# Optimization experiments

Measured on AMD Instinct MI355X. Metric: run time of the kernel, lower is better.

## Reference

```python
import jax, jax.numpy as jnp
import numpy as np

SOBEL_X = jnp.array([[-1., 0., 1.], [-2., 0., 2.], [-1., 0., 1.]], dtype=jnp.float32)
LAP = jnp.array([[1., 2., 1.], [2., -12., 2.], [1., 2., 1.]], dtype=jnp.float32)
UPDATE_RATE = 0.5


def _perchannel_conv(x, filters):
    # x: [B,C,H,W]; filters: [F,3,3]; circular pad, depthwise conv with F outputs per channel
    B, C, H, W = x.shape
    Fk = filters.shape[0]
    xp = jnp.pad(x, ((0, 0), (0, 0), (1, 1), (1, 1)), mode='wrap')
    # kernel[c*Fk + f] = filters[f] -> output channel order [c0f0,c0f1,c0f2,c1f0,...] matching torch reshape
    k = jnp.broadcast_to(filters[None], (C, Fk, 3, 3)).reshape(C * Fk, 1, 3, 3)
    return jax.lax.conv_general_dilated(xp, k, (1, 1), 'VALID',
                                        feature_group_count=C,
                                        dimension_numbers=('NCHW', 'OIHW', 'NCHW'))


def _unfold27(x):
    # circular pad over (C,H,W) then gather the 27-neighborhood: [B,C,H,W] -> [B,C,27,H,W]
    B, C, H, W = x.shape
    p = jnp.pad(x, ((0, 0), (1, 1), (1, 1), (1, 1)), mode='wrap')
    shifts = [p[:, dc:dc + C, dh:dh + H, dw:dw + W]
              for dc in range(3) for dh in range(3) for dw in range(3)]
    return jnp.stack(shifts, axis=2)


def setup_inputs() -> dict:
    key = jax.random.key(0)
    kx, km, k1, kb, k2 = jax.random.split(key, 5)
    B, C, H, W, HID = 4, 16, 512, 512, 128
    x = jax.random.normal(kx, (B, C, H, W), dtype=jnp.float32)
    rand_mask = jax.random.uniform(km, (B, 1, H, W), dtype=jnp.float32)
    w1_w = jax.random.normal(k1, (HID, 4 * C), dtype=jnp.float32) * 0.05
    w1_b = jax.random.normal(kb, (HID,), dtype=jnp.float32) * 0.05
    w2_w = jax.random.normal(k2, (C, HID), dtype=jnp.float32) * 0.05
    return {"x": x, "rand_mask": rand_mask, "w1_w": w1_w, "w1_b": w1_b, "w2_w": w2_w}


def reference(x, rand_mask, w1_w, w1_b, w2_w):
    filters = jnp.stack([SOBEL_X, SOBEL_X.T, LAP])  # [3,3,3]
    obs = _perchannel_conv(x, filters)              # [B,3C,H,W]
    percep = jnp.concatenate([x, obs], axis=1)      # [B,4C,H,W]
    h = jax.nn.relu(jnp.einsum('bchw,kc->bkhw', percep, w1_w) + w1_b[None, :, None, None])
    y = jnp.einsum('bkhw,ck->bchw', h, w2_w)        # [B,C,H,W]

    update_mask = jnp.floor(rand_mask + UPDATE_RATE)
    x_mass, x_normal = x[:, :3], x[:, 3:]
    y_mass, y_normal = y[:, :3], y[:, 3:]

    Aff = jnp.exp(y_mass * 0.1)                     # [B,3,H,W], strictly positive
    E = _unfold27(Aff).sum(axis=2)                  # total affinity of each cell's 27-neighborhood
    E_n = _unfold27(E)                              # neighbor normalizers
    S_n = _unfold27(x_mass)                         # neighbor masses
    new_mass = (Aff[:, :, None] / E_n * S_n).sum(axis=2)  # mass-conserving redistribution

    new_normal = x_normal + y_normal * update_mask
    return jnp.concatenate([new_mass, new_normal], axis=1)
```

## Files before the change

### kernel.cpp

```cpp
#include <hip/hip_runtime.h>

#define HW (512*512)
#define WMASK 511

typedef short bf16x8 __attribute__((ext_vector_type(8)));
typedef float f32x4 __attribute__((ext_vector_type(4)));
typedef unsigned int u32x4 __attribute__((ext_vector_type(4)));

__device__ __forceinline__ unsigned short f2bf(float f) {
    union { float f; unsigned int u; } v; v.f = f;
    unsigned int r = (v.u + 0x7FFFu + ((v.u >> 16) & 1u)) >> 16;
    return (unsigned short)r;
}
__device__ __forceinline__ unsigned int CVT(float lo, float hi) {
    unsigned int r;
    asm("v_cvt_pk_bf16_f32 %0, %1, %2" : "=v"(r) : "v"(lo), "v"(hi));
    return r;
}
__device__ __forceinline__ int corig(int c) {
    int s8 = c >> 3, b = (c >> 2) & 1, f = c & 3;
    int ch = 2*s8 + b;
    return (f == 0) ? ch : (16 + ch*3 + (f - 1));
}

__global__ __launch_bounds__(256) void nca_prep(
    const float* __restrict__ w1w, const float* __restrict__ w1b,
    const float* __restrict__ w2w, unsigned int* __restrict__ wbuf)
{
    int tid = threadIdx.x;
    for (int u = tid; u < 4096; u += 256) {
        int m2 = u >> 8, ln = (u >> 2) & 63, d = u & 3;
        int m = m2 >> 1, ks = m2 & 1;
        int qq = ln >> 4, row = ln & 15;
        int c0 = ks*32 + qq*8 + 2*d;
        int hr = m*16 + row;
        unsigned int lo = f2bf(w1w[hr*64 + corig(c0)]);
        unsigned int hi = f2bf(w1w[hr*64 + corig(c0+1)]);
        wbuf[u] = lo | (hi << 16);
    }
    for (int u = tid; u < 1024; u += 256) {
        int s = u >> 8, ln = (u >> 2) & 63, d = u & 3;
        int qq = ln >> 4, ych = ln & 15;
        int k0 = s*32 + qq*8 + 2*d;
        unsigned int lo = f2bf(w2w[ych*128 + k0]);
        unsigned int hi = f2bf(w2w[ych*128 + k0 + 1]);
        wbuf[4096 + u] = lo | (hi << 16);
    }
    if (tid < 128) {
        union { float f; unsigned int u; } v; v.f = w1b[tid];
        wbuf[5120 + tid] = v.u;
    }
}

__global__ __launch_bounds__(256) void nca_mlp_mfma(
    const float* __restrict__ x,
    const float* __restrict__ rmask,
    const unsigned int* __restrict__ wbuf,
    float* __restrict__ out,
    float* __restrict__ SA,
    float* __restrict__ SM)
{
    __shared__ __align__(16) unsigned int wsh[5248];
    __shared__ __align__(16) unsigned int hx[4][4][256];
    int tid  = threadIdx.x;
    int lane = tid & 63;
    int wv   = tid >> 6;
    int q    = lane >> 4;
    int r    = lane & 15;

    {
        const u32x4* src = (const u32x4*)wbuf;
        u32x4* dst = (u32x4*)wsh;
#pragma unroll
        for (int u = 0; u < 6; ++u) {
            int idx = tid + u*256;
            if (idx < 1312) dst[idx] = src[idx];
        }
    }

    int bIdx = blockIdx.x >> 10;
    int rem  = blockIdx.x & 1023;
    int hrow = ((rem >> 3) << 2) + wv;
    int w0   = (rem & 7) << 6;
    int c4   = w0 + (r << 2);
    int cl   = (c4 - 1) & WMASK;
    int cr   = (c4 + 4) & WMASK;
    int rm = ((hrow-1)&WMASK)<<9, rc = hrow<<9, rp = ((hrow+1)&WMASK)<<9;
    const float* xb = x + bIdx*16*HW;

    union PFU { unsigned int u[4]; bf16x8 v; } pf[4][2];
    f32x4 c_sav0, c_sav1;
#pragma unroll
    for (int ks = 0; ks < 2; ++ks) {
#pragma unroll
        for (int b2 = 0; b2 < 2; ++b2) {
            const float* pl = xb + (8*ks + 2*q + b2)*HW;
            f32x4 m0 = *(const f32x4*)(pl + rm + c4);
            f32x4 m1 = *(const f32x4*)(pl + rc + c4);
            f32x4 m2 = *(const f32x4*)(pl + rp + c4);
            if (ks == 0) { if (b2 == 0) c_sav0 = m1; else c_sav1 = m1; }
            float col[6][3];
            col[0][0] = pl[rm+cl]; col[0][1] = pl[rc+cl]; col[0][2] = pl[rp+cl];
#pragma unroll
            for (int j = 0; j < 4; ++j) {
                col[j+1][0] = m0[j]; col[j+1][1] = m1[j]; col[j+1][2] = m2[j];
            }
            col[5][0] = pl[rm+cr]; col[5][1] = pl[rc+cr]; col[5][2] = pl[rp+cr];
#pragma unroll
            for (int p = 0; p < 4; ++p) {
                float a00 = col[p][0],   a01 = col[p+1][0], a02 = col[p+2][0];
                float a10 = col[p][1],   a11 = col[p+1][1], a12 = col[p+2][1];
                float a20 = col[p][2],   a21 = col[p+1][2], a22 = col[p+2][2];
                float sx = (a02 - a00) + 2.f*(a12 - a10) + (a22 - a20);
                float sy = (a20 - a00) + 2.f*(a21 - a01) + (a22 - a02);
                float lp = a00 + 2.f*a01 + a02
                         + 2.f*a10 - 12.f*a11 + 2.f*a12
                         + a20 + 2.f*a21 + a22;
                pf[p][ks].u[2*b2]   = CVT(a11, sx);
                pf[p][ks].u[2*b2+1] = CVT(sy, lp);
            }
        }
    }

    __syncthreads();

    const unsigned short* w1s = (const unsigned short*)wsh;
    const unsigned short* w2s = (const unsigned short*)(wsh + 4096);
    const float* w1bs = (const float*)(wsh + 5120);

    unsigned int* hbase = &hx[wv][0][0];
    int k8a = (q >> 1);
    int k8b = 2 + (q >> 1);
    int wi0 = k8a*64 + ((r ^ k8a) << 2) + ((q & 1) << 1);
    int wi1 = k8b*64 + ((r ^ k8b) << 2) + ((q & 1) << 1);
    int ri  = q*64 + ((r ^ q) << 2);

    f32x4 yacc[4];
#pragma unroll
    for (int P = 0; P < 4; ++P) { yacc[P][0]=0.f; yacc[P][1]=0.f; yacc[P][2]=0.f; yacc[P][3]=0.f; }

#pragma unroll
    for (int s = 0; s < 4; ++s) {
        f32x4 Hc[2][4];
#pragma unroll
        for (int t = 0; t < 2; ++t)
#pragma unroll
            for (int P = 0; P < 4; ++P) { Hc[t][P][0]=0.f; Hc[t][P][1]=0.f; Hc[t][P][2]=0.f; Hc[t][P][3]=0.f; }

#pragma unroll
        for (int t = 0; t < 2; ++t) {
#pragma unroll
            for (int ks = 0; ks < 2; ++ks) {
                bf16x8 af = *(const bf16x8*)&w1s[(((2*s+t)*2 + ks)*64 + lane)*8];
#pragma unroll
                for (int P = 0; P < 4; ++P)
                    Hc[t][P] = __builtin_amdgcn_mfma_f32_16x16x32_bf16(af, pf[P][ks].v, Hc[t][P], 0, 0, 0);
            }
        }

        bf16x8 wf = *(const bf16x8*)&w2s[(s*64 + lane)*8];
        float bi0[2][4];
#pragma unroll
        for (int t = 0; t < 2; ++t) {
            const float* bp = &w1bs[(2*s+t)*16 + (q<<2)];
#pragma unroll
            for (int i = 0; i < 4; ++i) bi0[t][i] = bp[i];
        }

#pragma unroll
        for (int P = 0; P < 4; ++P) {
            unsigned int pk00, pk01, pk10, pk11;
            {
                f32x4 hv = Hc[0][P];
                float h0 = fmaxf(hv[0] + bi0[0][0], 0.f);
                float h1 = fmaxf(hv[1] + bi0[0][1], 0.f);
                float h2 = fmaxf(hv[2] + bi0[0][2], 0.f);
                float h3 = fmaxf(hv[3] + bi0[0][3], 0.f);
                pk00 = CVT(h0, h1); pk01 = CVT(h2, h3);
            }
            {
                f32x4 hv = Hc[1][P];
                float h0 = fmaxf(hv[0] + bi0[1][0], 0.f);
                float h1 = fmaxf(hv[1] + bi0[1][1], 0.f);
                float h2 = fmaxf(hv[2] + bi0[1][2], 0.f);
                float h3 = fmaxf(hv[3] + bi0[1][3], 0.f);
                pk10 = CVT(h0, h1); pk11 = CVT(h2, h3);
            }
            unsigned int* hb = hbase + P*256;
            *reinterpret_cast<unsigned long long*>(&hb[wi0]) =
                (unsigned long long)pk00 | ((unsigned long long)pk01 << 32);
            *reinterpret_cast<unsigned long long*>(&hb[wi1]) =
                (unsigned long long)pk10 | ((unsigned long long)pk11 << 32);
        }
#pragma unroll
        for (int P = 0; P < 4; ++P) {
            bf16x8 bv = *reinterpret_cast<const bf16x8*>(&hbase[P*256 + ri]);
            yacc[P] = __builtin_amdgcn_mfma_f32_16x16x32_bf16(wf, bv, yacc[P], 0, 0, 0);
        }
    }

    int pbase = rc + c4;
    f32x4 mk = *(const f32x4*)(rmask + bIdx*HW + pbase);
#pragma unroll
    for (int i = 0; i < 4; ++i) mk[i] = floorf(mk[i] + 0.5f);
    float* ob = out + bIdx*16*HW;

    if (q == 0) {
        f32x4 sacc;
#pragma unroll
        for (int i = 0; i < 3; ++i) {
            f32x4 A;
#pragma unroll
            for (int P = 0; P < 4; ++P) A[P] = expf(0.1f * yacc[P][i]);
            *(f32x4*)(ob + i*HW + pbase) = A;
            if (i == 0) sacc = A; else sacc += A;
        }
        *(f32x4*)(SA + bIdx*HW + pbase) = sacc;
        f32x4 x2v = *(const f32x4*)(xb + 2*HW + pbase);
        *(f32x4*)(SM + bIdx*HW + pbase) = c_sav0 + c_sav1 + x2v;
        f32x4 yv;
#pragma unroll
        for (int P = 0; P < 4; ++P) yv[P] = yacc[P][3];
        f32x4 xv = *(const f32x4*)(xb + 3*HW + pbase);
        *(f32x4*)(ob + 3*HW + pbase) = xv + yv*mk;
    } else {
#pragma unroll
        for (int i = 0; i < 4; ++i) {
            int ch = 4*q + i;
            f32x4 yv;
#pragma unroll
            for (int P = 0; P < 4; ++P) yv[P] = yacc[P][i];
            f32x4 xv = *(const f32x4*)(xb + ch*HW + pbase);
            *(f32x4*)(ob + ch*HW + pbase) = xv + yv*mk;
        }
    }
}

__global__ __launch_bounds__(256) void nca_bc(
    const float* __restrict__ SA,
    const float* __restrict__ SM,
    float* __restrict__ out)
{
    __shared__ float sa[12][69];
    __shared__ float tt[10][67];
    int tid = threadIdx.x;
    int bb = blockIdx.x >> 9;
    int t2 = blockIdx.x & 511;
    int h0 = (t2 >> 3) << 3;
    int w0 = (t2 & 7) << 6;
    const float* sab = SA + bb*HW;
    const float* smb = SM + bb*HW;

    for (int e = tid; e < 816; e += 256) {
        int rr = e / 68, cc = e - rr*68;
        int gh = (h0 + rr - 2) & WMASK, gw = (w0 + cc - 2) & WMASK;
        sa[rr][cc] = sab[(gh<<9) | gw];
    }
    __syncthreads();

    for (int e = tid; e < 660; e += 256) {
        int rr = e / 66, cc = e - rr*66;
        float E = sa[rr  ][cc] + sa[rr  ][cc+1] + sa[rr  ][cc+2]
                + sa[rr+1][cc] + sa[rr+1][cc+1] + sa[rr+1][cc+2]
                + sa[rr+2][cc] + sa[rr+2][cc+1] + sa[rr+2][cc+2];
        int gh = (h0 + rr - 1) & WMASK, gw = (w0 + cc - 1) & WMASK;
        int g = (gh<<9) | gw;
        tt[rr][cc] = smb[g] / E;
    }
    __syncthreads();

    for (int e = tid; e < 512; e += 256) {
        int rr = e >> 6, cc = e & 63;
        float R = tt[rr  ][cc] + tt[rr  ][cc+1] + tt[rr  ][cc+2]
                + tt[rr+1][cc] + tt[rr+1][cc+1] + tt[rr+1][cc+2]
                + tt[rr+2][cc] + tt[rr+2][cc+1] + tt[rr+2][cc+2];
        int p = ((h0 + rr) << 9) | (w0 + cc);
        float* ob = out + bb*16*HW + p;
        ob[0]    *= R;
        ob[HW]   *= R;
        ob[2*HW] *= R;
    }
}

extern "C" void kernel_launch(void* const* d_in, const int* in_sizes, int n_in,
                              void* d_out, int out_size, void* d_ws, size_t ws_size,
                              hipStream_t stream) {
    const float* x     = (const float*)d_in[0];
    const float* rmask = (const float*)d_in[1];
    const float* w1w   = (const float*)d_in[2];
    const float* w1b   = (const float*)d_in[3];
    const float* w2w   = (const float*)d_in[4];
    float* out = (float*)d_out;

    float* SA = (float*)d_ws;
    float* SM = SA + 4*HW;
    unsigned int* wbuf = (unsigned int*)((char*)d_ws + 8*HW*sizeof(float));

    hipLaunchKernelGGL(nca_prep,     dim3(1),    dim3(256), 0, stream, w1w, w1b, w2w, wbuf);
    hipLaunchKernelGGL(nca_mlp_mfma, dim3(4096), dim3(256), 0, stream, x, rmask, wbuf, out, SA, SM);
    hipLaunchKernelGGL(nca_bc,       dim3(2048), dim3(256), 0, stream, SA, SM, out);
}
```

Measured before the change: 184.1 us.

## Shrink hidden LDS staging, parallelize weight prep, use fast reciprocal

Several independent tweaks. The per-wave hidden-activation LDS buffer drops from four pixel groups to one, with each group written and read back in turn, which cuts shared memory and may raise occupancy but serializes the LDS round trips. The weight-prep kernel now runs across 21 blocks with one element per thread instead of one block looping, and bias loads become vectorized. The divide in the redistribution kernel is replaced with the hardware v_rcp_f32 approximation, which trades exact division for slightly lower precision.

```diff
diff --git a/kernel.cpp b/kernel.cpp
--- a/kernel.cpp
+++ b/kernel.cpp
@@ -17,6 +17,11 @@
     asm("v_cvt_pk_bf16_f32 %0, %1, %2" : "=v"(r) : "v"(lo), "v"(hi));
     return r;
 }
+__device__ __forceinline__ float RCP(float x) {
+    float r;
+    asm("v_rcp_f32 %0, %1" : "=v"(r) : "v"(x));
+    return r;
+}
 __device__ __forceinline__ int corig(int c) {
     int s8 = c >> 3, b = (c >> 2) & 1, f = c & 3;
     int ch = 2*s8 + b;
@@ -27,8 +32,8 @@
     const float* __restrict__ w1w, const float* __restrict__ w1b,
     const float* __restrict__ w2w, unsigned int* __restrict__ wbuf)
 {
-    int tid = threadIdx.x;
-    for (int u = tid; u < 4096; u += 256) {
+    int u = blockIdx.x * 256 + threadIdx.x;
+    if (u < 4096) {
         int m2 = u >> 8, ln = (u >> 2) & 63, d = u & 3;
         int m = m2 >> 1, ks = m2 & 1;
         int qq = ln >> 4, row = ln & 15;
@@ -37,18 +42,17 @@
         unsigned int lo = f2bf(w1w[hr*64 + corig(c0)]);
         unsigned int hi = f2bf(w1w[hr*64 + corig(c0+1)]);
         wbuf[u] = lo | (hi << 16);
-    }
-    for (int u = tid; u < 1024; u += 256) {
-        int s = u >> 8, ln = (u >> 2) & 63, d = u & 3;
+    } else if (u < 5120) {
+        int v = u - 4096;
+        int s = v >> 8, ln = (v >> 2) & 63, d = v & 3;
         int qq = ln >> 4, ych = ln & 15;
         int k0 = s*32 + qq*8 + 2*d;
         unsigned int lo = f2bf(w2w[ych*128 + k0]);
         unsigned int hi = f2bf(w2w[ych*128 + k0 + 1]);
-        wbuf[4096 + u] = lo | (hi << 16);
-    }
-    if (tid < 128) {
-        union { float f; unsigned int u; } v; v.f = w1b[tid];
-        wbuf[5120 + tid] = v.u;
+        wbuf[u] = lo | (hi << 16);
+    } else if (u < 5248) {
+        union { float f; unsigned int u; } v; v.f = w1b[u - 5120];
+        wbuf[u] = v.u;
     }
 }
 
@@ -61,7 +65,7 @@
     float* __restrict__ SM)
 {
     __shared__ __align__(16) unsigned int wsh[5248];
-    __shared__ __align__(16) unsigned int hx[4][4][256];
+    __shared__ __align__(16) unsigned int hx[4][256];
     int tid  = threadIdx.x;
     int lane = tid & 63;
     int wv   = tid >> 6;
@@ -128,7 +132,7 @@
     const unsigned short* w2s = (const unsigned short*)(wsh + 4096);
     const float* w1bs = (const float*)(wsh + 5120);
 
-    unsigned int* hbase = &hx[wv][0][0];
+    unsigned int* hbase = &hx[wv][0];
     int k8a = (q >> 1);
     int k8b = 2 + (q >> 1);
     int wi0 = k8a*64 + ((r ^ k8a) << 2) + ((q & 1) << 1);
@@ -159,42 +163,35 @@
         }
 
         bf16x8 wf = *(const bf16x8*)&w2s[(s*64 + lane)*8];
-        float bi0[2][4];
-#pragma unroll
-        for (int t = 0; t < 2; ++t) {
-            const float* bp = &w1bs[(2*s+t)*16 + (q<<2)];
-#pragma unroll
-            for (int i = 0; i < 4; ++i) bi0[t][i] = bp[i];
-        }
+        f32x4 bi[2];
+#pragma unroll
+        for (int t = 0; t < 2; ++t)
+            bi[t] = *(const f32x4*)&w1bs[(2*s+t)*16 + (q<<2)];
 
 #pragma unroll
         for (int P = 0; P < 4; ++P) {
             unsigned int pk00, pk01, pk10, pk11;
             {
                 f32x4 hv = Hc[0][P];
-                float h0 = fmaxf(hv[0] + bi0[0][0], 0.f);
-                float h1 = fmaxf(hv[1] + bi0[0][1], 0.f);
-                float h2 = fmaxf(hv[2] + bi0[0][2], 0.f);
-                float h3 = fmaxf(hv[3] + bi0[0][3], 0.f);
+                float h0 = fmaxf(hv[0] + bi[0][0], 0.f);
+                float h1 = fmaxf(hv[1] + bi[0][1], 0.f);
+                float h2 = fmaxf(hv[2] + bi[0][2], 0.f);
+                float h3 = fmaxf(hv[3] + bi[0][3], 0.f);
                 pk00 = CVT(h0, h1); pk01 = CVT(h2, h3);
             }
             {
                 f32x4 hv = Hc[1][P];
-                float h0 = fmaxf(hv[0] + bi0[1][0], 0.f);
-                float h1 = fmaxf(hv[1] + bi0[1][1], 0.f);
-                float h2 = fmaxf(hv[2] + bi0[1][2], 0.f);
-                float h3 = fmaxf(hv[3] + bi0[1][3], 0.f);
+                float h0 = fmaxf(hv[0] + bi[1][0], 0.f);
+                float h1 = fmaxf(hv[1] + bi[1][1], 0.f);
+                float h2 = fmaxf(hv[2] + bi[1][2], 0.f);
+                float h3 = fmaxf(hv[3] + bi[1][3], 0.f);
                 pk10 = CVT(h0, h1); pk11 = CVT(h2, h3);
             }
-            unsigned int* hb = hbase + P*256;
-            *reinterpret_cast<unsigned long long*>(&hb[wi0]) =
+            *reinterpret_cast<unsigned long long*>(&hbase[wi0]) =
                 (unsigned long long)pk00 | ((unsigned long long)pk01 << 32);
-            *reinterpret_cast<unsigned long long*>(&hb[wi1]) =
+            *reinterpret_cast<unsigned long long*>(&hbase[wi1]) =
                 (unsigned long long)pk10 | ((unsigned long long)pk11 << 32);
-        }
-#pragma unroll
-        for (int P = 0; P < 4; ++P) {
-            bf16x8 bv = *reinterpret_cast<const bf16x8*>(&hbase[P*256 + ri]);
+            bf16x8 bv = *reinterpret_cast<const bf16x8*>(&hbase[ri]);
             yacc[P] = __builtin_amdgcn_mfma_f32_16x16x32_bf16(wf, bv, yacc[P], 0, 0, 0);
         }
     }
@@ -265,7 +262,7 @@
                 + sa[rr+2][cc] + sa[rr+2][cc+1] + sa[rr+2][cc+2];
         int gh = (h0 + rr - 1) & WMASK, gw = (w0 + cc - 1) & WMASK;
         int g = (gh<<9) | gw;
-        tt[rr][cc] = smb[g] / E;
+        tt[rr][cc] = smb[g] * RCP(E);
     }
     __syncthreads();
 
@@ -296,7 +293,7 @@
     float* SM = SA + 4*HW;
     unsigned int* wbuf = (unsigned int*)((char*)d_ws + 8*HW*sizeof(float));
 
-    hipLaunchKernelGGL(nca_prep,     dim3(1),    dim3(256), 0, stream, w1w, w1b, w2w, wbuf);
+    hipLaunchKernelGGL(nca_prep,     dim3(21),   dim3(256), 0, stream, w1w, w1b, w2w, wbuf);
     hipLaunchKernelGGL(nca_mlp_mfma, dim3(4096), dim3(256), 0, stream, x, rmask, wbuf, out, SA, SM);
     hipLaunchKernelGGL(nca_bc,       dim3(2048), dim3(256), 0, stream, SA, SM, out);
 }
```

Measured after the change: 171.3 us. 7.0% less time.
